# Performance work log

Measured on AMD Instinct MI355X. Metric: run time of the kernel, lower is better.

## Reference

```python
import jax, jax.numpy as jnp
import numpy as np

B, LQ, LK, D = 32, 2048, 2048, 128
MASK_P = 0.1  # fraction of masked-out (True) positions


def setup_inputs() -> dict:
    key = jax.random.key(0)
    kq, kk, kv, km = jax.random.split(key, 4)
    q = jax.random.normal(kq, (B, LQ, D), dtype=jnp.float32)
    k = jax.random.normal(kk, (B, LK, D), dtype=jnp.float32)
    v = jax.random.normal(kv, (B, LK, D), dtype=jnp.float32)
    mask = jax.random.bernoulli(km, MASK_P, (B, LQ, LK))  # True = masked out
    return {"q": q, "k": k, "v": v, "mask": mask}


def reference(q, k, v, mask):
    # Faithful to the original: score is MULTIPLIED by sqrt(dk) (module's bug kept).
    dk = k.shape[-1]
    score = jnp.einsum('bqd,bkd->bqk', q, k) * jnp.sqrt(jnp.float32(dk))
    # masked_fill_(mask, -inf)
    score = jnp.where(mask, -jnp.inf, score)
    attn = jax.nn.softmax(score, axis=2)
    # torch.where(isnan(attn), 0, attn): fully-masked rows (all -inf) -> 0
    attn = jnp.where(jnp.isnan(attn), jnp.zeros_like(attn), attn)
    # dropout_rate = 0.0 -> identity
    context = jnp.einsum('bqk,bkd->bqd', attn, v)
    return context
```

## Files before the change

kernel.cpp:

```cpp
#include <hip/hip_runtime.h>
#include <math.h>

#define NB  32
#define NLQ 2048
#define NLK 2048
#define ND  128
#define KT  64
#define SCALE 11.3137084989847603904f

typedef float f32x4 __attribute__((ext_vector_type(4)));
typedef short s16x8 __attribute__((ext_vector_type(8)));
typedef unsigned short u16;
typedef unsigned short u16x8 __attribute__((ext_vector_type(8)));

__device__ int g_maskflag;

static __device__ __forceinline__ u16 f2bf(float x) {
    unsigned int u = __float_as_uint(x);
    return (u16)((u + 0x7FFFu + ((u >> 16) & 1u)) >> 16);
}
static __device__ __forceinline__ float bf2f(u16 b) {
    return __uint_as_float(((unsigned int)b) << 16);
}

#define SPLIT8(H, L, J, VAL) do { float _v = (VAL); u16 _hb = f2bf(_v); \
    (H)[J] = (short)_hb; (L)[J] = (short)f2bf(_v - bf2f(_hb)); } while (0)

#define GLDS(lds, src) __builtin_amdgcn_global_load_lds( \
    (const __attribute__((address_space(1))) unsigned int*)(src), \
    (__attribute__((address_space(3))) unsigned int*)(lds), 16, 0, 0)

__global__ void zero_flag_kernel() { if (threadIdx.x == 0) g_maskflag = 0; }

__global__ void detect_mask_kernel(const unsigned char* __restrict__ m) {
    unsigned int i = blockIdx.x * blockDim.x + threadIdx.x;
    bool nz = m[(size_t)i * 4 + 1] != 0;
    if (__any((int)nz) && (threadIdx.x & 63) == 0) atomicOr(&g_maskflag, 1);
}

__global__ void __launch_bounds__(256)
ksplit_kernel(const float* __restrict__ K, u16* __restrict__ Khi, u16* __restrict__ Klo) {
    int idx  = blockIdx.x * 256 + threadIdx.x;
    int d0   = (idx & 15) << 3;
    int krow = idx >> 4;
    const float* src = K + (size_t)krow * ND + d0;
    float4 x0 = *(const float4*)src;
    float4 x1 = *(const float4*)(src + 4);
    float xs[8] = {x0.x, x0.y, x0.z, x0.w, x1.x, x1.y, x1.z, x1.w};
    u16x8 h, l;
    #pragma unroll
    for (int j = 0; j < 8; ++j) { u16 hb = f2bf(xs[j]); h[j] = hb; l[j] = f2bf(xs[j] - bf2f(hb)); }
    int kkl = krow & 63;
    size_t tbase = ((size_t)(krow >> 6)) * 8192;
    int off = (kkl * ND + d0) ^ ((kkl & 7) << 3);
    *(u16x8*)(Khi + tbase + off) = h;
    *(u16x8*)(Klo + tbase + off) = l;
}

__global__ void __launch_bounds__(256)
vtrans_kernel(const float* __restrict__ V, u16* __restrict__ Vt) {
    int gw = (blockIdx.x * 256 + threadIdx.x) >> 6;
    int ln = threadIdx.x & 63;
    int dgrp = gw & 15;
    int tile = gw >> 4;
    int dl = ln >> 3, chunk = ln & 7;
    int d = dgrp * 8 + dl;
    int kk0 = chunk * 8;
    const float* src = V + ((size_t)tile * 64 + kk0) * ND + d;
    u16x8 o;
    #pragma unroll
    for (int j = 0; j < 8; ++j) o[j] = f2bf(src[(size_t)j * ND]);
    *(u16x8*)(Vt + (size_t)tile * 8192 + ((d * KT + kk0) ^ ((d & 7) << 3))) = o;
}

__global__ void __launch_bounds__(256, 2)
attn2_kernel(const float* __restrict__ Q, const unsigned char* __restrict__ Mb,
             float* __restrict__ Out,
             const u16* __restrict__ Khi, const u16* __restrict__ Klo,
             const u16* __restrict__ Vt)
{
    __shared__ u16 sKh[KT * ND];
    __shared__ u16 sKl[KT * ND];
    __shared__ u16 sVt[ND * KT];
    __shared__ u16 sP[4][2][16 * KT];

    const int tid  = threadIdx.x;
    const int wave = tid >> 6;
    const int ln   = tid & 63;
    const int g    = ln >> 4;
    const int qi   = ln & 15;

    const int n    = blockIdx.x;
    const int orig = ((n & 7) << 6) | (n >> 3);
    const int b    = orig >> 4;
    const int qt   = orig & 15;
    const int qbase = qt * 128 + wave * 32;

    const bool maskByte = (g_maskflag != 0);

    s16x8 qh8[2][4], ql8[2][4];
    #pragma unroll
    for (int u = 0; u < 2; ++u) {
        const float* qp = Q + ((size_t)b * NLQ + qbase + u * 16 + qi) * ND;
        #pragma unroll
        for (int c = 0; c < 4; ++c) {
            const float* p = qp + c * 32 + g * 8;
            float4 x0 = *(const float4*)(p);
            float4 x1 = *(const float4*)(p + 4);
            s16x8 h, l;
            SPLIT8(h, l, 0, x0.x * SCALE); SPLIT8(h, l, 1, x0.y * SCALE);
            SPLIT8(h, l, 2, x0.z * SCALE); SPLIT8(h, l, 3, x0.w * SCALE);
            SPLIT8(h, l, 4, x1.x * SCALE); SPLIT8(h, l, 5, x1.y * SCALE);
            SPLIT8(h, l, 6, x1.z * SCALE); SPLIT8(h, l, 7, x1.w * SCALE);
            qh8[u][c] = h; ql8[u][c] = l;
        }
    }

    f32x4 o[2][8];
    #pragma unroll
    for (int u = 0; u < 2; ++u)
        #pragma unroll
        for (int t = 0; t < 8; ++t) o[u][t] = (f32x4){0.f, 0.f, 0.f, 0.f};
    float mrun[2] = {-INFINITY, -INFINITY}, lsum[2] = {0.f, 0.f};

    const size_t mrow0 = ((size_t)b * NLQ + qbase + qi) * (size_t)NLK;
    const size_t mrow1 = mrow0 + (size_t)16 * NLK;

    const u16* khT = Khi + (size_t)b * 32 * 8192;
    const u16* klT = Klo + (size_t)b * 32 * 8192;
    const u16* vtT = Vt  + (size_t)b * 32 * 8192;

    for (int kt = 0; kt < NLK / KT; ++kt) {
        const int kb = kt * KT;
        __syncthreads();

        {
            const char* s0 = (const char*)(khT + (size_t)kt * 8192) + (size_t)wave * 1024 + (size_t)ln * 16;
            const char* s1 = (const char*)(klT + (size_t)kt * 8192) + (size_t)wave * 1024 + (size_t)ln * 16;
            const char* s2 = (const char*)(vtT + (size_t)kt * 8192) + (size_t)wave * 1024 + (size_t)ln * 16;
            #pragma unroll
            for (int i = 0; i < 4; ++i) {
                GLDS(&sKh[i * 2048 + wave * 512], s0 + i * 4096);
                GLDS(&sKl[i * 2048 + wave * 512], s1 + i * 4096);
                GLDS(&sVt[i * 2048 + wave * 512], s2 + i * 4096);
            }
        }

        unsigned mbitsA[2];
        if (maskByte) {
            #pragma unroll
            for (int u = 0; u < 2; ++u) {
                size_t mrow = u ? mrow1 : mrow0;
                unsigned bits = 0;
                #pragma unroll
                for (int s = 0; s < 4; ++s) {
                    unsigned mm = *(const unsigned*)(Mb + mrow + (size_t)(kb + s * 16 + 4 * g));
                    #pragma unroll
                    for (int j = 0; j < 4; ++j)
                        bits |= (((mm >> (8 * j)) & 0xFFu) ? 1u : 0u) << (s * 4 + j);
                }
                mbitsA[u] = bits;
            }
        } else {
            const int* Mi = (const int*)Mb;
            #pragma unroll
            for (int u = 0; u < 2; ++u) {
                size_t mrow = u ? mrow1 : mrow0;
                unsigned bits = 0;
                #pragma unroll
                for (int s = 0; s < 4; ++s) {
                    int4 mm = *(const int4*)(Mi + mrow + (size_t)(kb + s * 16 + 4 * g));
                    if (mm.x) bits |= 1u << (s * 4 + 0);
                    if (mm.y) bits |= 1u << (s * 4 + 1);
                    if (mm.z) bits |= 1u << (s * 4 + 2);
                    if (mm.w) bits |= 1u << (s * 4 + 3);
                }
                mbitsA[u] = bits;
            }
        }
        __syncthreads();

        float p[2][16];
        #pragma unroll
        for (int s = 0; s < 4; ++s) {
            f32x4 a0 = (f32x4){0.f, 0.f, 0.f, 0.f};
            f32x4 a1 = (f32x4){0.f, 0.f, 0.f, 0.f};
            int row = s * 16 + qi;
            int rowoff = row * ND, swz = (row & 7) << 3;
            #pragma unroll
            for (int c = 0; c < 4; ++c) {
                int off = (rowoff + c * 32 + g * 8) ^ swz;
                s16x8 kh = *(s16x8*)&sKh[off];
                s16x8 kl = *(s16x8*)&sKl[off];
                a0 = __builtin_amdgcn_mfma_f32_16x16x32_bf16(kh, qh8[0][c], a0, 0, 0, 0);
                a1 = __builtin_amdgcn_mfma_f32_16x16x32_bf16(kh, qh8[1][c], a1, 0, 0, 0);
                a0 = __builtin_amdgcn_mfma_f32_16x16x32_bf16(kh, ql8[0][c], a0, 0, 0, 0);
                a1 = __builtin_amdgcn_mfma_f32_16x16x32_bf16(kh, ql8[1][c], a1, 0, 0, 0);
                a0 = __builtin_amdgcn_mfma_f32_16x16x32_bf16(kl, qh8[0][c], a0, 0, 0, 0);
                a1 = __builtin_amdgcn_mfma_f32_16x16x32_bf16(kl, qh8[1][c], a1, 0, 0, 0);
            }
            #pragma unroll
            for (int r = 0; r < 4; ++r) { p[0][s * 4 + r] = a0[r]; p[1][s * 4 + r] = a1[r]; }
        }

        #pragma unroll
        for (int u = 0; u < 2; ++u) {
            unsigned mbits = mbitsA[u];
            float tmax = -INFINITY;
            #pragma unroll
            for (int i = 0; i < 16; ++i) {
                float sv = ((mbits >> i) & 1u) ? -INFINITY : p[u][i];
                p[u][i] = sv;
                tmax = fmaxf(tmax, sv);
            }
            tmax = fmaxf(tmax, __shfl_xor(tmax, 16));
            tmax = fmaxf(tmax, __shfl_xor(tmax, 32));
            float mnew = fmaxf(mrun[u], tmax);
            float corr = (mnew == -INFINITY) ? 0.f : __expf(mrun[u] - mnew);
            float psum = 0.f;
            #pragma unroll
            for (int i = 0; i < 16; ++i) {
                float pv = ((mbits >> i) & 1u) ? 0.f : __expf(p[u][i] - mnew);
                p[u][i] = pv;
                psum += pv;
            }
            psum += __shfl_xor(psum, 16);
            psum += __shfl_xor(psum, 32);
            lsum[u] = lsum[u] * corr + psum;
            mrun[u] = mnew;
            #pragma unroll
            for (int j = 0; j < 4; ++j) {
                float cj = __shfl(corr, 4 * g + j, 64);
                #pragma unroll
                for (int t = 0; t < 8; ++t) o[u][t][j] *= cj;
            }
            #pragma unroll
            for (int s = 0; s < 4; ++s) {
                ushort4 p4;
                p4.x = f2bf(p[u][s * 4 + 0]); p4.y = f2bf(p[u][s * 4 + 1]);
                p4.z = f2bf(p[u][s * 4 + 2]); p4.w = f2bf(p[u][s * 4 + 3]);
                int off = (qi * KT + s * 16 + 4 * g) ^ ((qi & 7) << 3);
                *(ushort4*)&sP[wave][u][off] = p4;
            }
        }

        #pragma unroll
        for (int h = 0; h < 2; ++h) {
            int offp = (qi * KT + h * 32 + g * 8) ^ ((qi & 7) << 3);
            s16x8 pa0 = *(s16x8*)&sP[wave][0][offp];
            s16x8 pa1 = *(s16x8*)&sP[wave][1][offp];
            #pragma unroll
            for (int t = 0; t < 8; ++t) {
                int d = t * 16 + qi;
                int offv = (d * KT + h * 32 + g * 8) ^ ((d & 7) << 3);
                s16x8 vb = *(s16x8*)&sVt[offv];
                o[0][t] = __builtin_amdgcn_mfma_f32_16x16x32_bf16(pa0, vb, o[0][t], 0, 0, 0);
                o[1][t] = __builtin_amdgcn_mfma_f32_16x16x32_bf16(pa1, vb, o[1][t], 0, 0, 0);
            }
        }
    }

    #pragma unroll
    for (int u = 0; u < 2; ++u)
        #pragma unroll
        for (int j = 0; j < 4; ++j) {
            float lj = __shfl(lsum[u], 4 * g + j, 64);
            float inv = (lj > 0.f) ? (1.0f / lj) : 0.f;
            int row = qbase + u * 16 + 4 * g + j;
            float* op = Out + ((size_t)b * NLQ + row) * ND + qi;
            #pragma unroll
            for (int t = 0; t < 8; ++t) op[t * 16] = o[u][t][j] * inv;
        }
}

__global__ void __launch_bounds__(256, 2)
attn_fallback(const float* __restrict__ Q, const float* __restrict__ K,
              const float* __restrict__ V, const unsigned char* __restrict__ Mb,
              float* __restrict__ Out)
{
    __shared__ u16 sKh[KT * ND];
    __shared__ u16 sKl[KT * ND];
    __shared__ u16 sVt[ND * KT];
    __shared__ u16 sP[4][16 * KT];

    const int tid  = threadIdx.x;
    const int wave = tid >> 6;
    const int ln   = tid & 63;
    const int g    = ln >> 4;
    const int qi   = ln & 15;

    const int bid   = blockIdx.x;
    const int b     = bid >> 5;
    const int qt    = bid & 31;
    const int qbase = qt * 64;
    const int qrow  = qbase + wave * 16 + qi;

    const bool maskByte = (g_maskflag != 0);

    s16x8 qh8[4], ql8[4];
    {
        const float* qp = Q + ((size_t)b * NLQ + qrow) * ND;
        #pragma unroll
        for (int c = 0; c < 4; ++c) {
            const float* p = qp + c * 32 + g * 8;
            float4 x0 = *(const float4*)(p);
            float4 x1 = *(const float4*)(p + 4);
            s16x8 h, l;
            SPLIT8(h, l, 0, x0.x * SCALE); SPLIT8(h, l, 1, x0.y * SCALE);
            SPLIT8(h, l, 2, x0.z * SCALE); SPLIT8(h, l, 3, x0.w * SCALE);
            SPLIT8(h, l, 4, x1.x * SCALE); SPLIT8(h, l, 5, x1.y * SCALE);
            SPLIT8(h, l, 6, x1.z * SCALE); SPLIT8(h, l, 7, x1.w * SCALE);
            qh8[c] = h; ql8[c] = l;
        }
    }

    f32x4 o[8];
    #pragma unroll
    for (int t = 0; t < 8; ++t) o[t] = (f32x4){0.f, 0.f, 0.f, 0.f};
    float m_run = -INFINITY, lsumv = 0.f;

    const float* kbp = K + (size_t)b * NLK * ND;
    const float* vbp = V + (size_t)b * NLK * ND;
    const size_t mrow = ((size_t)b * NLQ + qrow) * (size_t)NLK;

    for (int kt = 0; kt < NLK / KT; ++kt) {
        const int kb = kt * KT;
        __syncthreads();

        #pragma unroll
        for (int r = 0; r < 8; ++r) {
            int idx = r * 256 + tid;
            int kk  = idx >> 5;
            int d0  = (idx & 31) << 2;
            float4 x = *(const float4*)(kbp + (size_t)(kb + kk) * ND + d0);
            ushort4 h4, l4; u16 hb;
            hb = f2bf(x.x); h4.x = hb; l4.x = f2bf(x.x - bf2f(hb));
            hb = f2bf(x.y); h4.y = hb; l4.y = f2bf(x.y - bf2f(hb));
            hb = f2bf(x.z); h4.z = hb; l4.z = f2bf(x.z - bf2f(hb));
            hb = f2bf(x.w); h4.w = hb; l4.w = f2bf(x.w - bf2f(hb));
            int off = (kk * ND + d0) ^ ((kk & 7) << 3);
            *(ushort4*)&sKh[off] = h4;
            *(ushort4*)&sKl[off] = l4;
        }
        #pragma unroll
        for (int r = 0; r < 2; ++r) {
            int idx = r * 256 + tid;
            int kk0 = (idx >> 5) << 2;
            int d0  = (idx & 31) << 2;
            const float* vp = vbp + (size_t)(kb + kk0) * ND + d0;
            float4 r0 = *(const float4*)(vp);
            float4 r1 = *(const float4*)(vp + ND);
            float4 r2 = *(const float4*)(vp + 2 * ND);
            float4 r3 = *(const float4*)(vp + 3 * ND);
            ushort4 cv;
            cv.x = f2bf(r0.x); cv.y = f2bf(r1.x); cv.z = f2bf(r2.x); cv.w = f2bf(r3.x);
            { int d = d0;     *(ushort4*)&sVt[(d * KT + kk0) ^ ((d & 7) << 3)] = cv; }
            cv.x = f2bf(r0.y); cv.y = f2bf(r1.y); cv.z = f2bf(r2.y); cv.w = f2bf(r3.y);
            { int d = d0 + 1; *(ushort4*)&sVt[(d * KT + kk0) ^ ((d & 7) << 3)] = cv; }
            cv.x = f2bf(r0.z); cv.y = f2bf(r1.z); cv.z = f2bf(r2.z); cv.w = f2bf(r3.z);
            { int d = d0 + 2; *(ushort4*)&sVt[(d * KT + kk0) ^ ((d & 7) << 3)] = cv; }
            cv.x = f2bf(r0.w); cv.y = f2bf(r1.w); cv.z = f2bf(r2.w); cv.w = f2bf(r3.w);
            { int d = d0 + 3; *(ushort4*)&sVt[(d * KT + kk0) ^ ((d & 7) << 3)] = cv; }
        }
        __syncthreads();

        unsigned maskbits = 0;
        if (maskByte) {
            #pragma unroll
            for (int s = 0; s < 4; ++s) {
                unsigned mm = *(const unsigned int*)(Mb + mrow + (size_t)(kb + s * 16 + 4 * g));
                #pragma unroll
                for (int j = 0; j < 4; ++j)
                    maskbits |= (((mm >> (8 * j)) & 0xFFu) ? 1u : 0u) << (s * 4 + j);
            }
        } else {
            const int* Mi = (const int*)Mb;
            #pragma unroll
            for (int s = 0; s < 4; ++s) {
                int4 mm = *(const int4*)(Mi + mrow + (size_t)(kb + s * 16 + 4 * g));
                if (mm.x) maskbits |= 1u << (s * 4 + 0);
                if (mm.y) maskbits |= 1u << (s * 4 + 1);
                if (mm.z) maskbits |= 1u << (s * 4 + 2);
                if (mm.w) maskbits |= 1u << (s * 4 + 3);
            }
        }

        float p[16];
        #pragma unroll
        for (int s = 0; s < 4; ++s) {
            f32x4 acc = (f32x4){0.f, 0.f, 0.f, 0.f};
            int rowoff = (s * 16 + qi) * ND;
            int swz = ((s * 16 + qi) & 7) << 3;
            #pragma unroll
            for (int c = 0; c < 4; ++c) {
                int off = (rowoff + c * 32 + g * 8) ^ swz;
                s16x8 kh = *(s16x8*)&sKh[off];
                s16x8 kl = *(s16x8*)&sKl[off];
                acc = __builtin_amdgcn_mfma_f32_16x16x32_bf16(kh, qh8[c], acc, 0, 0, 0);
                acc = __builtin_amdgcn_mfma_f32_16x16x32_bf16(kh, ql8[c], acc, 0, 0, 0);
                acc = __builtin_amdgcn_mfma_f32_16x16x32_bf16(kl, qh8[c], acc, 0, 0, 0);
            }
            p[s * 4 + 0] = acc[0]; p[s * 4 + 1] = acc[1];
            p[s * 4 + 2] = acc[2]; p[s * 4 + 3] = acc[3];
        }

        float tmax = -INFINITY;
        #pragma unroll
        for (int i = 0; i < 16; ++i) {
            float sv = ((maskbits >> i) & 1u) ? -INFINITY : p[i];
            p[i] = sv;
            tmax = fmaxf(tmax, sv);
        }
        tmax = fmaxf(tmax, __shfl_xor(tmax, 16));
        tmax = fmaxf(tmax, __shfl_xor(tmax, 32));
        float mnew = fmaxf(m_run, tmax);
        float corr = (mnew == -INFINITY) ? 0.f : __expf(m_run - mnew);
        float psum = 0.f;
        #pragma unroll
        for (int i = 0; i < 16; ++i) {
            float pv = ((maskbits >> i) & 1u) ? 0.f : __expf(p[i] - mnew);
            p[i] = pv;
            psum += pv;
        }
        psum += __shfl_xor(psum, 16);
        psum += __shfl_xor(psum, 32);
        lsumv = lsumv * corr + psum;
        m_run = mnew;

        #pragma unroll
        for (int j = 0; j < 4; ++j) {
            float cj = __shfl(corr, 4 * g + j, 64);
            #pragma unroll
            for (int t = 0; t < 8; ++t) o[t][j] *= cj;
        }

        #pragma unroll
        for (int s = 0; s < 4; ++s) {
            ushort4 p4;
            p4.x = f2bf(p[s * 4 + 0]); p4.y = f2bf(p[s * 4 + 1]);
            p4.z = f2bf(p[s * 4 + 2]); p4.w = f2bf(p[s * 4 + 3]);
            int off = (qi * KT + s * 16 + 4 * g) ^ ((qi & 7) << 3);
            *(ushort4*)&sP[wave][off] = p4;
        }
        #pragma unroll
        for (int h = 0; h < 2; ++h) {
            int offp = (qi * KT + h * 32 + g * 8) ^ ((qi & 7) << 3);
            s16x8 pa = *(s16x8*)&sP[wave][offp];
            #pragma unroll
            for (int t = 0; t < 8; ++t) {
                int d = t * 16 + qi;
                int offv = (d * KT + h * 32 + g * 8) ^ ((d & 7) << 3);
                s16x8 vb = *(s16x8*)&sVt[offv];
                o[t] = __builtin_amdgcn_mfma_f32_16x16x32_bf16(pa, vb, o[t], 0, 0, 0);
            }
        }
    }

    #pragma unroll
    for (int j = 0; j < 4; ++j) {
        float lj = __shfl(lsumv, 4 * g + j, 64);
        float inv = (lj > 0.f) ? (1.0f / lj) : 0.f;
        int row = qbase + wave * 16 + 4 * g + j;
        float* op = Out + ((size_t)b * NLQ + row) * ND + qi;
        #pragma unroll
        for (int t = 0; t < 8; ++t) op[t * 16] = o[t][j] * inv;
    }
}

extern "C" void kernel_launch(void* const* d_in, const int* in_sizes, int n_in,
                              void* d_out, int out_size, void* d_ws, size_t ws_size,
                              hipStream_t stream) {
    (void)in_sizes; (void)n_in; (void)out_size;
    const float* Q = (const float*)d_in[0];
    const float* K = (const float*)d_in[1];
    const float* V = (const float*)d_in[2];
    const unsigned char* M = (const unsigned char*)d_in[3];
    float* Out = (float*)d_out;

    zero_flag_kernel<<<1, 64, 0, stream>>>();
    detect_mask_kernel<<<64, 256, 0, stream>>>(M);

    const size_t WS_NEED = (size_t)48 * 1024 * 1024;
    if (ws_size >= WS_NEED) {
        u16* Khi = (u16*)d_ws;
        u16* Klo = Khi + 8388608;
        u16* Vt  = Klo + 8388608;
        ksplit_kernel<<<4096, 256, 0, stream>>>(K, Khi, Klo);
        vtrans_kernel<<<4096, 256, 0, stream>>>(V, Vt);
        attn2_kernel<<<512, 256, 0, stream>>>(Q, M, Out, Khi, Klo, Vt);
    } else {
        attn_fallback<<<1024, 256, 0, stream>>>(Q, K, V, M, Out);
    }
}
```

Baseline: 1.006 ms.

## Prepack mask bits, double-buffer K/V tiles, use 512-thread blocks with lazy rescale

Adds a pre-pass that packs the mask into 64-bit bitwords with ballots, so the attention kernel reads one word per row per tile instead of bytes or ints. The new kernel runs 8 waves per block, double-buffers K-hi/K-lo/Vt tiles in 128KB of dynamic LDS so the next tile loads while the current one is computed, and keeps one barrier per iteration. Softmax moves to exp2 with log2e folded into the Q scale, and it skips the output rescale when the running max rises by at most 8. This costs an extra pass over the mask and more LDS per block, which may lower occupancy.

```diff
diff --git a/kernel.cpp b/kernel.cpp
--- a/kernel.cpp
+++ b/kernel.cpp
@@ -6,12 +6,14 @@
 #define NLK 2048
 #define ND  128
 #define KT  64
-#define SCALE 11.3137084989847603904f
+#define SCALE2 16.3231239813435843f
+#define SCALE  11.3137084989847603904f
 
 typedef float f32x4 __attribute__((ext_vector_type(4)));
 typedef short s16x8 __attribute__((ext_vector_type(8)));
 typedef unsigned short u16;
 typedef unsigned short u16x8 __attribute__((ext_vector_type(8)));
+typedef unsigned long long u64;
 
 __device__ int g_maskflag;
 
@@ -36,6 +38,30 @@
     unsigned int i = blockIdx.x * blockDim.x + threadIdx.x;
     bool nz = m[(size_t)i * 4 + 1] != 0;
     if (__any((int)nz) && (threadIdx.x & 63) == 0) atomicOr(&g_maskflag, 1);
+}
+
+__global__ void __launch_bounds__(256)
+maskbits_kernel(const unsigned char* __restrict__ M, u64* __restrict__ Bits) {
+    const size_t NWORDS = (size_t)NB * NLQ * (NLK / 64);
+    const int ln = threadIdx.x & 63;
+    const size_t wgid = ((size_t)blockIdx.x * 256 + threadIdx.x) >> 6;
+    const size_t NW = (size_t)4096 * 4;
+    if (g_maskflag != 0) {
+        #pragma unroll 4
+        for (size_t w = wgid; w < NWORDS; w += NW) {
+            unsigned char v = M[w * 64 + ln];
+            u64 bal = __ballot(v != 0);
+            if (ln == 0) Bits[w] = bal;
+        }
+    } else {
+        const int* Mi = (const int*)M;
+        #pragma unroll 4
+        for (size_t w = wgid; w < NWORDS; w += NW) {
+            int v = Mi[w * 64 + ln];
+            u64 bal = __ballot(v != 0);
+            if (ln == 0) Bits[w] = bal;
+        }
+    }
 }
 
 __global__ void __launch_bounds__(256)
@@ -73,16 +99,16 @@
     *(u16x8*)(Vt + (size_t)tile * 8192 + ((d * KT + kk0) ^ ((d & 7) << 3))) = o;
 }
 
-__global__ void __launch_bounds__(256, 2)
-attn2_kernel(const float* __restrict__ Q, const unsigned char* __restrict__ Mb,
+__global__ void __launch_bounds__(512, 2)
+attn3_kernel(const float* __restrict__ Q, const u64* __restrict__ Bits,
              float* __restrict__ Out,
              const u16* __restrict__ Khi, const u16* __restrict__ Klo,
              const u16* __restrict__ Vt)
 {
-    __shared__ u16 sKh[KT * ND];
-    __shared__ u16 sKl[KT * ND];
-    __shared__ u16 sVt[ND * KT];
-    __shared__ u16 sP[4][2][16 * KT];
+    extern __shared__ u16 smem[];
+    u16* bufA = smem;
+    u16* bufB = smem + 24576;
+    u16* sPb  = smem + 49152;
 
     const int tid  = threadIdx.x;
     const int wave = tid >> 6;
@@ -91,12 +117,10 @@
     const int qi   = ln & 15;
 
     const int n    = blockIdx.x;
-    const int orig = ((n & 7) << 6) | (n >> 3);
-    const int b    = orig >> 4;
-    const int qt   = orig & 15;
-    const int qbase = qt * 128 + wave * 32;
-
-    const bool maskByte = (g_maskflag != 0);
+    const int orig = ((n & 7) << 5) | (n >> 3);
+    const int b    = orig >> 3;
+    const int qt   = orig & 7;
+    const int qbase = qt * 256 + wave * 32;
 
     s16x8 qh8[2][4], ql8[2][4];
     #pragma unroll
@@ -108,10 +132,10 @@
             float4 x0 = *(const float4*)(p);
             float4 x1 = *(const float4*)(p + 4);
             s16x8 h, l;
-            SPLIT8(h, l, 0, x0.x * SCALE); SPLIT8(h, l, 1, x0.y * SCALE);
-            SPLIT8(h, l, 2, x0.z * SCALE); SPLIT8(h, l, 3, x0.w * SCALE);
-            SPLIT8(h, l, 4, x1.x * SCALE); SPLIT8(h, l, 5, x1.y * SCALE);
-            SPLIT8(h, l, 6, x1.z * SCALE); SPLIT8(h, l, 7, x1.w * SCALE);
+            SPLIT8(h, l, 0, x0.x * SCALE2); SPLIT8(h, l, 1, x0.y * SCALE2);
+            SPLIT8(h, l, 2, x0.z * SCALE2); SPLIT8(h, l, 3, x0.w * SCALE2);
+            SPLIT8(h, l, 4, x1.x * SCALE2); SPLIT8(h, l, 5, x1.y * SCALE2);
+            SPLIT8(h, l, 6, x1.z * SCALE2); SPLIT8(h, l, 7, x1.w * SCALE2);
             qh8[u][c] = h; ql8[u][c] = l;
         }
     }
@@ -122,63 +146,45 @@
         #pragma unroll
         for (int t = 0; t < 8; ++t) o[u][t] = (f32x4){0.f, 0.f, 0.f, 0.f};
     float mrun[2] = {-INFINITY, -INFINITY}, lsum[2] = {0.f, 0.f};
-
-    const size_t mrow0 = ((size_t)b * NLQ + qbase + qi) * (size_t)NLK;
-    const size_t mrow1 = mrow0 + (size_t)16 * NLK;
 
     const u16* khT = Khi + (size_t)b * 32 * 8192;
     const u16* klT = Klo + (size_t)b * 32 * 8192;
     const u16* vtT = Vt  + (size_t)b * 32 * 8192;
 
-    for (int kt = 0; kt < NLK / KT; ++kt) {
-        const int kb = kt * KT;
-        __syncthreads();
-
-        {
-            const char* s0 = (const char*)(khT + (size_t)kt * 8192) + (size_t)wave * 1024 + (size_t)ln * 16;
-            const char* s1 = (const char*)(klT + (size_t)kt * 8192) + (size_t)wave * 1024 + (size_t)ln * 16;
-            const char* s2 = (const char*)(vtT + (size_t)kt * 8192) + (size_t)wave * 1024 + (size_t)ln * 16;
-            #pragma unroll
-            for (int i = 0; i < 4; ++i) {
-                GLDS(&sKh[i * 2048 + wave * 512], s0 + i * 4096);
-                GLDS(&sKl[i * 2048 + wave * 512], s1 + i * 4096);
-                GLDS(&sVt[i * 2048 + wave * 512], s2 + i * 4096);
-            }
-        }
-
-        unsigned mbitsA[2];
-        if (maskByte) {
-            #pragma unroll
-            for (int u = 0; u < 2; ++u) {
-                size_t mrow = u ? mrow1 : mrow0;
-                unsigned bits = 0;
-                #pragma unroll
-                for (int s = 0; s < 4; ++s) {
-                    unsigned mm = *(const unsigned*)(Mb + mrow + (size_t)(kb + s * 16 + 4 * g));
-                    #pragma unroll
-                    for (int j = 0; j < 4; ++j)
-                        bits |= (((mm >> (8 * j)) & 0xFFu) ? 1u : 0u) << (s * 4 + j);
-                }
-                mbitsA[u] = bits;
-            }
-        } else {
-            const int* Mi = (const int*)Mb;
-            #pragma unroll
-            for (int u = 0; u < 2; ++u) {
-                size_t mrow = u ? mrow1 : mrow0;
-                unsigned bits = 0;
-                #pragma unroll
-                for (int s = 0; s < 4; ++s) {
-                    int4 mm = *(const int4*)(Mi + mrow + (size_t)(kb + s * 16 + 4 * g));
-                    if (mm.x) bits |= 1u << (s * 4 + 0);
-                    if (mm.y) bits |= 1u << (s * 4 + 1);
-                    if (mm.z) bits |= 1u << (s * 4 + 2);
-                    if (mm.w) bits |= 1u << (s * 4 + 3);
-                }
-                mbitsA[u] = bits;
-            }
-        }
-        __syncthreads();
+    const size_t row0 = (size_t)b * NLQ + qbase + qi;
+    const u64* bw0 = Bits + row0 * 32;
+    const u64* bw1 = Bits + (row0 + 16) * 32;
+
+#define STAGE_TILE(dst, kt_) do { \
+    const char* _sK = (const char*)(khT + (size_t)(kt_) * 8192) + wave * 2048 + ln * 16; \
+    const char* _sL = (const char*)(klT + (size_t)(kt_) * 8192) + wave * 2048 + ln * 16; \
+    const char* _sV = (const char*)(vtT + (size_t)(kt_) * 8192) + wave * 2048 + ln * 16; \
+    GLDS((dst) + wave * 1024,               _sK); \
+    GLDS((dst) + wave * 1024 + 512,         _sK + 1024); \
+    GLDS((dst) + 8192  + wave * 1024,       _sL); \
+    GLDS((dst) + 8192  + wave * 1024 + 512, _sL + 1024); \
+    GLDS((dst) + 16384 + wave * 1024,       _sV); \
+    GLDS((dst) + 16384 + wave * 1024 + 512, _sV + 1024); \
+} while (0)
+
+    STAGE_TILE(bufA, 0);
+    u64 mw0 = bw0[0], mw1 = bw1[0];
+    __syncthreads();
+
+    u16* cur = bufA;
+    u16* nxt = bufB;
+
+    for (int kt = 0; kt < 32; ++kt) {
+        u64 nmw0 = mw0, nmw1 = mw1;
+        if (kt < 31) {
+            STAGE_TILE(nxt, kt + 1);
+            nmw0 = bw0[kt + 1];
+            nmw1 = bw1[kt + 1];
+        }
+
+        u16* sKh = cur;
+        u16* sKl = cur + 8192;
+        u16* sVt_ = cur + 16384;
 
         float p[2][16];
         #pragma unroll
@@ -205,59 +211,81 @@
 
         #pragma unroll
         for (int u = 0; u < 2; ++u) {
-            unsigned mbits = mbitsA[u];
-            float tmax = -INFINITY;
+            u64 mw = u ? mw1 : mw0;
+            unsigned mbits = 0;
+            #pragma unroll
+            for (int s = 0; s < 4; ++s)
+                mbits |= (unsigned)((mw >> (s * 16 + 4 * g)) & 0xFull) << (4 * s);
+
+            float tm = -INFINITY;
             #pragma unroll
             for (int i = 0; i < 16; ++i) {
                 float sv = ((mbits >> i) & 1u) ? -INFINITY : p[u][i];
                 p[u][i] = sv;
-                tmax = fmaxf(tmax, sv);
-            }
-            tmax = fmaxf(tmax, __shfl_xor(tmax, 16));
-            tmax = fmaxf(tmax, __shfl_xor(tmax, 32));
-            float mnew = fmaxf(mrun[u], tmax);
-            float corr = (mnew == -INFINITY) ? 0.f : __expf(mrun[u] - mnew);
+                tm = fmaxf(tm, sv);
+            }
+            tm = fmaxf(tm, __shfl_xor(tm, 16));
+            tm = fmaxf(tm, __shfl_xor(tm, 32));
+
+            float mold = mrun[u];
+            bool defer = (mold > -INFINITY) && __all((int)(tm <= mold + 8.f));
+            float m_use = mold;
+            if (!defer) {
+                float mnew = fmaxf(mold, tm);
+                float corr = (mnew == -INFINITY) ? 0.f : __builtin_exp2f(mold - mnew);
+                lsum[u] *= corr;
+                #pragma unroll
+                for (int j = 0; j < 4; ++j) {
+                    float cj = __shfl(corr, 4 * g + j, 64);
+                    #pragma unroll
+                    for (int t = 0; t < 8; ++t) o[u][t][j] *= cj;
+                }
+                mrun[u] = mnew;
+                m_use = mnew;
+            }
+
             float psum = 0.f;
             #pragma unroll
             for (int i = 0; i < 16; ++i) {
-                float pv = ((mbits >> i) & 1u) ? 0.f : __expf(p[u][i] - mnew);
+                float pv = ((mbits >> i) & 1u) ? 0.f : __builtin_exp2f(p[u][i] - m_use);
                 p[u][i] = pv;
                 psum += pv;
             }
             psum += __shfl_xor(psum, 16);
             psum += __shfl_xor(psum, 32);
-            lsum[u] = lsum[u] * corr + psum;
-            mrun[u] = mnew;
-            #pragma unroll
-            for (int j = 0; j < 4; ++j) {
-                float cj = __shfl(corr, 4 * g + j, 64);
-                #pragma unroll
-                for (int t = 0; t < 8; ++t) o[u][t][j] *= cj;
-            }
+            lsum[u] += psum;
+
+            u16* sP = sPb + (wave * 2 + u) * 1024;
             #pragma unroll
             for (int s = 0; s < 4; ++s) {
                 ushort4 p4;
                 p4.x = f2bf(p[u][s * 4 + 0]); p4.y = f2bf(p[u][s * 4 + 1]);
                 p4.z = f2bf(p[u][s * 4 + 2]); p4.w = f2bf(p[u][s * 4 + 3]);
                 int off = (qi * KT + s * 16 + 4 * g) ^ ((qi & 7) << 3);
-                *(ushort4*)&sP[wave][u][off] = p4;
-            }
-        }
-
+                *(ushort4*)&sP[off] = p4;
+            }
+        }
+
+        u16* sP0 = sPb + (wave * 2 + 0) * 1024;
+        u16* sP1 = sPb + (wave * 2 + 1) * 1024;
         #pragma unroll
         for (int h = 0; h < 2; ++h) {
             int offp = (qi * KT + h * 32 + g * 8) ^ ((qi & 7) << 3);
-            s16x8 pa0 = *(s16x8*)&sP[wave][0][offp];
-            s16x8 pa1 = *(s16x8*)&sP[wave][1][offp];
+            s16x8 pa0 = *(s16x8*)&sP0[offp];
+            s16x8 pa1 = *(s16x8*)&sP1[offp];
             #pragma unroll
             for (int t = 0; t < 8; ++t) {
                 int d = t * 16 + qi;
                 int offv = (d * KT + h * 32 + g * 8) ^ ((d & 7) << 3);
-                s16x8 vb = *(s16x8*)&sVt[offv];
+                s16x8 vb = *(s16x8*)&sVt_[offv];
                 o[0][t] = __builtin_amdgcn_mfma_f32_16x16x32_bf16(pa0, vb, o[0][t], 0, 0, 0);
                 o[1][t] = __builtin_amdgcn_mfma_f32_16x16x32_bf16(pa1, vb, o[1][t], 0, 0, 0);
             }
         }
+
+        __syncthreads();
+        mw0 = nmw0; mw1 = nmw1;
+        u16* tswap = cur; cur = nxt; nxt = tswap;
     }
 
     #pragma unroll
@@ -271,6 +299,7 @@
             #pragma unroll
             for (int t = 0; t < 8; ++t) op[t * 16] = o[u][t][j] * inv;
         }
+#undef STAGE_TILE
 }
 
 __global__ void __launch_bounds__(256, 2)
@@ -480,14 +509,18 @@
     zero_flag_kernel<<<1, 64, 0, stream>>>();
     detect_mask_kernel<<<64, 256, 0, stream>>>(M);
 
-    const size_t WS_NEED = (size_t)48 * 1024 * 1024;
+    const size_t WS_NEED = (size_t)64 * 1024 * 1024;
     if (ws_size >= WS_NEED) {
         u16* Khi = (u16*)d_ws;
         u16* Klo = Khi + 8388608;
         u16* Vt  = Klo + 8388608;
+        u64* Bits = (u64*)(Vt + 8388608);
+        maskbits_kernel<<<4096, 256, 0, stream>>>(M, Bits);
         ksplit_kernel<<<4096, 256, 0, stream>>>(K, Khi, Klo);
         vtrans_kernel<<<4096, 256, 0, stream>>>(V, Vt);
-        attn2_kernel<<<512, 256, 0, stream>>>(Q, M, Out, Khi, Klo, Vt);
+        hipFuncSetAttribute((const void*)attn3_kernel,
+                            hipFuncAttributeMaxDynamicSharedMemorySize, 131072);
+        attn3_kernel<<<256, 512, 131072, stream>>>(Q, Bits, Out, Khi, Klo, Vt);
     } else {
         attn_fallback<<<1024, 256, 0, stream>>>(Q, K, V, M, Out);
     }
```

New measurement: 964.2 us. 1.04x faster.
